# Performance work log

Hardware: AMD Instinct MI355X
Metric: run time of the kernel (lower is better)

Reference implementation:

```python
import jax, jax.numpy as jnp
import numpy as np

N, E, DIN, DOUT, DE = 100000, 250000, 32, 32, 13


def setup_inputs() -> dict:
    key = jax.random.key(0)
    ks = jax.random.split(key, 10)
    def u(k, shape, fan):
        b = 1.0 / np.sqrt(fan)
        return jax.random.uniform(k, shape, jnp.float32, -b, b)
    x = jax.random.normal(ks[0], (N, DIN), jnp.float32)
    edge_index = jax.random.randint(ks[1], (2, E), 0, N)
    edge_attr = jax.random.uniform(ks[2], (E, DE), jnp.float32)
    # NNConv's edge network: Linear(DE -> DIN*DOUT)
    nn_w = u(ks[3], (DIN * DOUT, DE), DE)
    nn_b = u(ks[4], (DIN * DOUT,), DE)
    # NNConv root weight + bias
    root = u(ks[5], (DIN, DOUT), DIN)
    bias = jnp.zeros((DOUT,), jnp.float32)
    # GRU(input=DIN, hidden=DOUT), single layer, seq_len=1
    w_ih = u(ks[6], (3 * DOUT, DIN), DOUT)
    w_hh = u(ks[7], (3 * DOUT, DOUT), DOUT)
    b_ih = u(ks[8], (3 * DOUT,), DOUT)
    b_hh = u(ks[9], (3 * DOUT,), DOUT)
    return dict(x=x, edge_attr=edge_attr, nn_w=nn_w, nn_b=nn_b, root=root,
                bias=bias, w_ih=w_ih, w_hh=w_hh, b_ih=b_ih, b_hh=b_hh,
                edge_index=edge_index)


def reference(x, edge_attr, nn_w, nn_b, root, bias, w_ih, w_hh, b_ih, b_hh, edge_index):
    identity = x
    h0 = x  # h is None -> h = x.unsqueeze(0); squeeze the seq dim here
    # norm='_None' (identity) and Dropout in eval mode (identity)
    src, dst = edge_index[0], edge_index[1]
    # NNConv: per-edge weight matrix from edge_attr  [E, DIN, DOUT]
    W = (edge_attr @ nn_w.T + nn_b).reshape(E, DIN, DOUT)
    msg = jnp.einsum('ei,eio->eo', x[src], W)           # [E, DOUT]
    agg = jax.ops.segment_sum(msg, dst, num_segments=N)  # [N, DOUT]
    cnt = jax.ops.segment_sum(jnp.ones((E, 1), x.dtype), dst, num_segments=N)
    mean = agg / jnp.maximum(cnt, 1.0)                   # aggr='mean'
    conv = mean + x @ root + bias
    # celu then GRU step (seq_len=1)
    c = jax.nn.celu(conv)
    gi = c @ w_ih.T + b_ih
    gh = h0 @ w_hh.T + b_hh
    ir, iz, ic = jnp.split(gi, 3, axis=1)
    hr, hz, hc = jnp.split(gh, 3, axis=1)
    r = jax.nn.sigmoid(ir + hr)
    z = jax.nn.sigmoid(iz + hz)
    n = jnp.tanh(ic + r * hc)
    h_new = (1.0 - z) * n + z * h0
    out = jax.nn.relu(h_new + identity)  # res=True, act=ReLU
    return out, h_new[None]
```

## Files before the change

kernel.cpp:

```cpp
#include <hip/hip_runtime.h>
#include <hip/hip_bf16.h>
#include <stdint.h>

#define DIN 32
#define DOUT 32
#define DE 13

typedef float f32x4 __attribute__((ext_vector_type(4)));
typedef short s16x8 __attribute__((ext_vector_type(8)));
typedef int   i32x4 __attribute__((ext_vector_type(4)));

__device__ __forceinline__ float bf2f(unsigned short u) {
    return __uint_as_float(((uint32_t)u) << 16);
}
__device__ __forceinline__ unsigned short f2bf(float f) {
    uint32_t b = __float_as_uint(f);
    b += 0x7FFFu + ((b >> 16) & 1u);
    return (unsigned short)(b >> 16);
}
__device__ __forceinline__ uint32_t pk2(float a, float b) {
    float2 t; t.x = a; t.y = b;
    __hip_bfloat162 h = __float22bfloat162_rn(t);
    return *(uint32_t*)&h;
}
__device__ __forceinline__ float sigm(float v) { return 1.f / (1.f + __expf(-v)); }
__device__ __forceinline__ float tanh_fast(float v) { return 2.f / (1.f + __expf(-2.f * v)) - 1.f; }

#define KE_LDS (28 * 512)
__global__ __launch_bounds__(256) void kE(const float* __restrict__ x,
        const float* __restrict__ ea, const int* __restrict__ ei,
        const float* __restrict__ nn_w, const float* __restrict__ nn_b,
        __hip_bfloat162* __restrict__ agg, float* __restrict__ cnt, int E) {
    __shared__ unsigned short Al[KE_LDS];
    __shared__ uint32_t tr4[4][256];
    const int tid = threadIdx.x;
    for (int t = tid; t < KE_LDS; t += 256) {
        int j = t & 7;
        int lane = (t >> 3) & 63;
        int tile = t >> 9;
        int at2 = tile >= 14 ? 1 : 0;
        int kt = tile - at2 * 14;
        int o = at2 * 16 + (lane & 15);
        int i = ((lane >> 4) << 3) + j;
        float v = (kt < 13) ? nn_w[(i * 32 + o) * 13 + kt] : nn_b[i * 32 + o];
        Al[t] = f2bf(v);
    }
    __syncthreads();
    const int lane = tid & 63;
    const int wv = tid >> 6;
    const int el = lane & 15;
    const int quad = lane >> 4;
    const int q8 = quad << 3;
    uint32_t* trw = &tr4[wv][0];
    const int wave = (blockIdx.x * 256 + tid) >> 6;
    const int nw = (gridDim.x * 256) >> 6;
    const int nstrips = E >> 4;
    for (int s = wave; s < nstrips; s += nw) {
        const int e = (s << 4) + el;
        const int srcv = ei[e];
        const int dstv = ei[E + e];
        const float* eab = ea + (size_t)(s << 4) * 13;
        #pragma unroll
        for (int t = 0; t < 4; ++t) {
            int idx = t * 64 + lane;
            if (idx < 208) trw[idx] = __float_as_uint(eab[idx]);
        }
        const float* xq = x + (size_t)srcv * 32 + q8;
        f32x4 xlo = *(const f32x4*)xq;
        f32x4 xhi = *(const f32x4*)(xq + 4);
        i32x4 bi;
        bi[0] = pk2(xlo[0], xlo[1]);
        bi[1] = pk2(xlo[2], xlo[3]);
        bi[2] = pk2(xhi[0], xhi[1]);
        bi[3] = pk2(xhi[2], xhi[3]);
        s16x8 bfr = __builtin_bit_cast(s16x8, bi);
        float g[14];
        #pragma unroll
        for (int d = 0; d < 13; ++d) g[d] = __uint_as_float(trw[el * 13 + d]);
        g[13] = 1.0f;
        f32x4 acc0 = {0.f, 0.f, 0.f, 0.f}, acc1 = {0.f, 0.f, 0.f, 0.f};
        const f32x4 zz = {0.f, 0.f, 0.f, 0.f};
        #pragma unroll
        for (int kt = 0; kt < 14; ++kt) {
            s16x8 a0 = *(const s16x8*)&Al[kt * 512 + lane * 8];
            s16x8 a1 = *(const s16x8*)&Al[(14 + kt) * 512 + lane * 8];
            f32x4 y0 = __builtin_amdgcn_mfma_f32_16x16x32_bf16(a0, bfr, zz, 0, 0, 0);
            f32x4 y1 = __builtin_amdgcn_mfma_f32_16x16x32_bf16(a1, bfr, zz, 0, 0, 0);
            float gk = g[kt];
            #pragma unroll
            for (int r = 0; r < 4; ++r) {
                acc0[r] = fmaf(gk, y0[r], acc0[r]);
                acc1[r] = fmaf(gk, y1[r], acc1[r]);
            }
        }
        {
            uint2 p0, p1;
            p0.x = pk2(acc0[0], acc0[1]); p0.y = pk2(acc0[2], acc0[3]);
            p1.x = pk2(acc1[0], acc1[1]); p1.y = pk2(acc1[2], acc1[3]);
            *(uint2*)&trw[el * 16 + quad * 2] = p0;
            *(uint2*)&trw[el * 16 + 8 + quad * 2] = p1;
        }
        #pragma unroll
        for (int p = 0; p < 4; ++p) {
            int e4 = (p << 2) + quad;
            uint32_t val = trw[e4 * 16 + el];
            int d4 = __shfl(dstv, e4, 64);
            __hip_bfloat162 hv = *(__hip_bfloat162*)&val;
            unsafeAtomicAdd(&agg[(size_t)d4 * 16 + el], hv);
        }
        if (lane < 16) atomicAdd(&cnt[dstv], 1.0f);
    }
}

__global__ __launch_bounds__(256) void kF(const float* __restrict__ x,
        const __hip_bfloat16* __restrict__ aggb, const float* __restrict__ cnt,
        const float* __restrict__ root, const float* __restrict__ bias,
        const float* __restrict__ w_ih, const float* __restrict__ w_hh,
        const float* __restrict__ b_ih, const float* __restrict__ b_hh,
        float* __restrict__ out, float* __restrict__ hnew, int N) {
    __shared__ __align__(16) char smem[30720];
    unsigned short* Bl = (unsigned short*)smem;
    float* scr = (float*)(smem + 14336);
    unsigned short* clds = (unsigned short*)(smem + 14336);
    const int tid = threadIdx.x;
    {
        *(f32x4*)&scr[tid * 4] = *(const f32x4*)&root[tid * 4];
        #pragma unroll
        for (int it = 0; it < 3; ++it)
            *(f32x4*)&scr[1024 + it * 1024 + tid * 4] =
                *(const f32x4*)&w_ih[0 * 0 + it * 1024 + tid * 4 - 0 * 0] * 0.f +
                *(const f32x4*)&w_hh[it * 1024 + tid * 4];
    }
    __syncthreads();
    for (int t = tid; t < 8 * 512; t += 256) {
        int j = t & 7;
        int ln = (t >> 3) & 63;
        int tt = t >> 9;
        int i = ((ln >> 4) << 3) + j;
        int c = ln & 15;
        int col = tt * 16 + c;
        float v = (col < 32) ? scr[i * 32 + col] : scr[1024 + (col - 32) * 32 + i];
        Bl[t] = f2bf(v);
    }
    __syncthreads();
    #pragma unroll
    for (int it = 0; it < 3; ++it)
        *(f32x4*)&scr[it * 1024 + tid * 4] = *(const f32x4*)&w_ih[it * 1024 + tid * 4];
    __syncthreads();
    for (int t = tid + 8 * 512; t < 14 * 512; t += 256) {
        int j = t & 7;
        int ln = (t >> 3) & 63;
        int tt = t >> 9;
        int i = ((ln >> 4) << 3) + j;
        int c = ln & 15;
        Bl[t] = f2bf(scr[((tt - 8) * 16 + c) * 32 + i]);
    }
    __syncthreads();
    const int lane = tid & 63;
    const int wv = tid >> 6;
    const int c15 = lane & 15;
    const int rowb = (lane >> 4) << 2;
    unsigned short* cl = clds + wv * 512;
    float binit[14];
    #pragma unroll
    for (int t = 0; t < 2; ++t) binit[t] = bias[t * 16 + c15];
    #pragma unroll
    for (int t = 2; t < 8; ++t) binit[t] = b_hh[t * 16 + c15 - 32];
    #pragma unroll
    for (int u = 0; u < 6; ++u) binit[8 + u] = b_ih[u * 16 + c15];
    int wave = (blockIdx.x * 256 + tid) >> 6;
    const int nw = (gridDim.x * 256) >> 6;
    const int nstrips = N >> 4;
    for (int s = wave; s < nstrips; s += nw) {
        const int n0 = s << 4;
        const float* xp = x + (size_t)(n0 + c15) * 32 + ((lane >> 4) << 3);
        f32x4 x0 = *(const f32x4*)xp;
        f32x4 x1 = *(const f32x4*)(xp + 4);
        float xr[4][2], ag[4][2], cn[4];
        #pragma unroll
        for (int r = 0; r < 4; ++r) {
            const int n = n0 + rowb + r;
            cn[r] = cnt[n];
            #pragma unroll
            for (int t = 0; t < 2; ++t) {
                xr[r][t] = x[(size_t)n * 32 + t * 16 + c15];
                ag[r][t] = bf2f(*(const unsigned short*)&aggb[(size_t)n * 32 + t * 16 + c15]);
            }
        }
        s16x8 a;
        a[0] = (short)f2bf(x0[0]); a[1] = (short)f2bf(x0[1]);
        a[2] = (short)f2bf(x0[2]); a[3] = (short)f2bf(x0[3]);
        a[4] = (short)f2bf(x1[0]); a[5] = (short)f2bf(x1[1]);
        a[6] = (short)f2bf(x1[2]); a[7] = (short)f2bf(x1[3]);
        f32x4 D[8];
        #pragma unroll
        for (int t = 0; t < 8; ++t) {
            s16x8 b = *(const s16x8*)&Bl[(t * 64 + lane) * 8];
            f32x4 ci = {binit[t], binit[t], binit[t], binit[t]};
            D[t] = __builtin_amdgcn_mfma_f32_16x16x32_bf16(a, b, ci, 0, 0, 0);
        }
        #pragma unroll
        for (int r = 0; r < 4; ++r) {
            float icn = 1.f / fmaxf(cn[r], 1.f);
            #pragma unroll
            for (int t = 0; t < 2; ++t) {
                float conv = ag[r][t] * icn + D[t][r];
                float cv = conv > 0.f ? conv : (__expf(conv) - 1.f);
                cl[(rowb + r) * 32 + t * 16 + c15] = f2bf(cv);
            }
        }
        s16x8 a2 = *(const s16x8*)&cl[c15 * 32 + ((lane >> 4) << 3)];
        f32x4 G[6];
        #pragma unroll
        for (int u = 0; u < 6; ++u) {
            s16x8 b = *(const s16x8*)&Bl[((8 + u) * 64 + lane) * 8];
            f32x4 ci = {binit[8 + u], binit[8 + u], binit[8 + u], binit[8 + u]};
            G[u] = __builtin_amdgcn_mfma_f32_16x16x32_bf16(a2, b, ci, 0, 0, 0);
        }
        #pragma unroll
        for (int t = 0; t < 2; ++t) {
            #pragma unroll
            for (int r = 0; r < 4; ++r) {
                float rg = sigm(G[t][r] + D[2 + t][r]);
                float z  = sigm(G[2 + t][r] + D[4 + t][r]);
                float nn = tanh_fast(G[4 + t][r] + rg * D[6 + t][r]);
                float h  = (1.f - z) * nn + z * xr[r][t];
                float ov = h + xr[r][t];
                size_t oi = (size_t)(n0 + rowb + r) * 32 + t * 16 + c15;
                out[oi]  = ov > 0.f ? ov : 0.f;
                hnew[oi] = h;
            }
        }
    }
}

extern "C" void kernel_launch(void* const* d_in, const int* in_sizes, int n_in,
                              void* d_out, int out_size, void* d_ws, size_t ws_size,
                              hipStream_t stream) {
    const float* x    = (const float*)d_in[0];
    const float* ea   = (const float*)d_in[1];
    const float* nn_w = (const float*)d_in[2];
    const float* nn_b = (const float*)d_in[3];
    const float* root = (const float*)d_in[4];
    const float* bias = (const float*)d_in[5];
    const float* w_ih = (const float*)d_in[6];
    const float* w_hh = (const float*)d_in[7];
    const float* b_ih = (const float*)d_in[8];
    const float* b_hh = (const float*)d_in[9];
    const int*   ei   = (const int*)d_in[10];
    const int N = in_sizes[0] / DIN;
    const int E = in_sizes[10] / 2;
    float* out  = (float*)d_out;
    float* hnew = out + (size_t)N * DOUT;

    const size_t agg_bytes = (size_t)N * 32 * sizeof(__hip_bfloat16);

    __hip_bfloat162* agg = (__hip_bfloat162*)d_ws;
    float* cnt = (float*)((char*)d_ws + agg_bytes);
    kE<<<1024, 256, 0, stream>>>(x, ea, ei, nn_w, nn_b, agg, cnt, E);
    kF<<<768, 256, 0, stream>>>(x, (const __hip_bfloat16*)d_ws, cnt, root, bias,
                                w_ih, w_hh, b_ih, b_hh, out, hnew, N);
}
```

Measured before the change: 146.6 us.

## Replicate scatter accumulators per XCC and reduce replicas in the node kernel

The edge kernel reads the hardware XCC id and sends its bf16 aggregate and count atomics into a per-XCC replica of the accumulator buffers. It issues them as raw non-returning global atomics, which keeps each atomic inside the local XCC's L2 instead of contending across dies. The node kernel then sums all 8 replicas when it loads each node's aggregate and count. The packed layout changes so the two halves of the output pair into one 32-bit word. This trades eight times the workspace and extra reads in the node kernel for less cross-die atomic traffic, and falls back to a single replica if the workspace is too small.

```diff
diff --git a/kernel.cpp b/kernel.cpp
--- a/kernel.cpp
+++ b/kernel.cpp
@@ -9,6 +9,7 @@
 typedef float f32x4 __attribute__((ext_vector_type(4)));
 typedef short s16x8 __attribute__((ext_vector_type(8)));
 typedef int   i32x4 __attribute__((ext_vector_type(4)));
+typedef unsigned int u32x4 __attribute__((ext_vector_type(4)));
 
 __device__ __forceinline__ float bf2f(unsigned short u) {
     return __uint_as_float(((uint32_t)u) << 16);
@@ -27,13 +28,25 @@
 __device__ __forceinline__ float tanh_fast(float v) { return 2.f / (1.f + __expf(-2.f * v)) - 1.f; }
 
 #define KE_LDS (28 * 512)
+template<bool LOCAL>
 __global__ __launch_bounds__(256) void kE(const float* __restrict__ x,
         const float* __restrict__ ea, const int* __restrict__ ei,
         const float* __restrict__ nn_w, const float* __restrict__ nn_b,
-        __hip_bfloat162* __restrict__ agg, float* __restrict__ cnt, int E) {
+        uint32_t* __restrict__ agg, float* __restrict__ cnt, int E, int N) {
     __shared__ unsigned short Al[KE_LDS];
     __shared__ uint32_t tr4[4][256];
     const int tid = threadIdx.x;
+
+    uint32_t* aggx = agg;
+    float*    cntx = cnt;
+    if (LOCAL) {
+        uint32_t xcc;
+        asm("s_getreg_b32 %0, hwreg(HW_REG_XCC_ID)" : "=s"(xcc));
+        xcc &= 7u;
+        aggx = agg + (size_t)xcc * ((size_t)N * 16);
+        cntx = cnt + (size_t)xcc * (size_t)N;
+    }
+
     for (int t = tid; t < KE_LDS; t += 256) {
         int j = t & 7;
         int lane = (t >> 3) & 63;
@@ -94,26 +107,45 @@
             }
         }
         {
-            uint2 p0, p1;
-            p0.x = pk2(acc0[0], acc0[1]); p0.y = pk2(acc0[2], acc0[3]);
-            p1.x = pk2(acc1[0], acc1[1]); p1.y = pk2(acc1[2], acc1[3]);
-            *(uint2*)&trw[el * 16 + quad * 2] = p0;
-            *(uint2*)&trw[el * 16 + 8 + quad * 2] = p1;
+            u32x4 pw;
+            pw[0] = pk2(acc0[0], acc1[0]);
+            pw[1] = pk2(acc0[1], acc1[1]);
+            pw[2] = pk2(acc0[2], acc1[2]);
+            pw[3] = pk2(acc0[3], acc1[3]);
+            *(u32x4*)&trw[el * 16 + quad * 4] = pw;
         }
         #pragma unroll
         for (int p = 0; p < 4; ++p) {
             int e4 = (p << 2) + quad;
             uint32_t val = trw[e4 * 16 + el];
             int d4 = __shfl(dstv, e4, 64);
-            __hip_bfloat162 hv = *(__hip_bfloat162*)&val;
-            unsafeAtomicAdd(&agg[(size_t)d4 * 16 + el], hv);
-        }
-        if (lane < 16) atomicAdd(&cnt[dstv], 1.0f);
-    }
-}
-
+            if (LOCAL) {
+                uint32_t* pa = aggx + (size_t)d4 * 16 + el;
+                asm volatile("global_atomic_pk_add_bf16 %0, %1, off"
+                             :: "v"(pa), "v"(val) : "memory");
+            } else {
+                __hip_bfloat162 hv = *(__hip_bfloat162*)&val;
+                unsafeAtomicAdd((__hip_bfloat162*)(aggx + (size_t)d4 * 16 + el), hv);
+            }
+        }
+        if (lane < 16) {
+            if (LOCAL) {
+                float* pc = cntx + dstv;
+                asm volatile("global_atomic_add_f32 %0, %1, off"
+                             :: "v"(pc), "v"(1.0f) : "memory");
+            } else {
+                atomicAdd(&cntx[dstv], 1.0f);
+            }
+        }
+    }
+    if (LOCAL) {
+        asm volatile("s_waitcnt vmcnt(0)" ::: "memory");
+    }
+}
+
+template<int NREP>
 __global__ __launch_bounds__(256) void kF(const float* __restrict__ x,
-        const __hip_bfloat16* __restrict__ aggb, const float* __restrict__ cnt,
+        const uint32_t* __restrict__ aggw, const float* __restrict__ cnt,
         const float* __restrict__ root, const float* __restrict__ bias,
         const float* __restrict__ w_ih, const float* __restrict__ w_hh,
         const float* __restrict__ b_ih, const float* __restrict__ b_hh,
@@ -178,14 +210,26 @@
         f32x4 x1 = *(const f32x4*)(xp + 4);
         float xr[4][2], ag[4][2], cn[4];
         #pragma unroll
+        for (int r = 0; r < 4; ++r) { ag[r][0] = 0.f; ag[r][1] = 0.f; cn[r] = 0.f; }
+        #pragma unroll
+        for (int q = 0; q < NREP; ++q) {
+            const uint32_t* aw = aggw + (size_t)q * ((size_t)N * 16);
+            const float* cq = cnt + (size_t)q * N;
+            #pragma unroll
+            for (int r = 0; r < 4; ++r) {
+                const int n = n0 + rowb + r;
+                uint32_t w = aw[(size_t)n * 16 + c15];
+                ag[r][0] += bf2f((unsigned short)(w & 0xFFFFu));
+                ag[r][1] += bf2f((unsigned short)(w >> 16));
+                cn[r] += cq[n];
+            }
+        }
+        #pragma unroll
         for (int r = 0; r < 4; ++r) {
             const int n = n0 + rowb + r;
-            cn[r] = cnt[n];
-            #pragma unroll
-            for (int t = 0; t < 2; ++t) {
+            #pragma unroll
+            for (int t = 0; t < 2; ++t)
                 xr[r][t] = x[(size_t)n * 32 + t * 16 + c15];
-                ag[r][t] = bf2f(*(const unsigned short*)&aggb[(size_t)n * 32 + t * 16 + c15]);
-            }
         }
         s16x8 a;
         a[0] = (short)f2bf(x0[0]); a[1] = (short)f2bf(x0[1]);
@@ -253,11 +297,20 @@
     float* out  = (float*)d_out;
     float* hnew = out + (size_t)N * DOUT;
 
-    const size_t agg_bytes = (size_t)N * 32 * sizeof(__hip_bfloat16);
-
-    __hip_bfloat162* agg = (__hip_bfloat162*)d_ws;
-    float* cnt = (float*)((char*)d_ws + agg_bytes);
-    kE<<<1024, 256, 0, stream>>>(x, ea, ei, nn_w, nn_b, agg, cnt, E);
-    kF<<<768, 256, 0, stream>>>(x, (const __hip_bfloat16*)d_ws, cnt, root, bias,
-                                w_ih, w_hh, b_ih, b_hh, out, hnew, N);
-}
+    const size_t aggB = (size_t)N * 16 * sizeof(uint32_t);
+    const size_t cntB = (size_t)N * sizeof(float);
+    const bool rep8 = ws_size >= 8 * (aggB + cntB);
+    const int nrep = rep8 ? 8 : 1;
+
+    uint32_t* agg = (uint32_t*)d_ws;
+    float* cnt = (float*)((char*)d_ws + (size_t)nrep * aggB);
+    if (rep8) {
+        kE<true><<<1024, 256, 0, stream>>>(x, ea, ei, nn_w, nn_b, agg, cnt, E, N);
+        kF<8><<<768, 256, 0, stream>>>(x, agg, cnt, root, bias,
+                                       w_ih, w_hh, b_ih, b_hh, out, hnew, N);
+    } else {
+        kE<false><<<1024, 256, 0, stream>>>(x, ea, ei, nn_w, nn_b, agg, cnt, E, N);
+        kF<1><<<768, 256, 0, stream>>>(x, agg, cnt, root, bias,
+                                       w_ih, w_hh, b_ih, b_hh, out, hnew, N);
+    }
+}
```

Result: slower. 168.7 us (+15.1%).

## Software-pipeline edge kernel with double-buffered LDS and prefetched indices/features

Applied to the files above, without the earlier changes.

Restructures the edge kernel loop into a software pipeline. Edge indices are fetched two strips ahead, edge attributes one strip ahead through registers into a double-buffered LDS slot, and the next strip's source features are loaded before the atomics are issued. The bias tile now seeds the accumulators instead of running through the FMA loop, and the aggregate is packed so each bf16x2 word holds columns c and c+16. The node kernel reads that word with a single 32-bit load. Launch bounds add an occupancy hint and the node kernel grid grows; the extra registers and LDS could cut occupancy.

```diff
diff --git a/kernel.cpp b/kernel.cpp
--- a/kernel.cpp
+++ b/kernel.cpp
@@ -9,6 +9,7 @@
 typedef float f32x4 __attribute__((ext_vector_type(4)));
 typedef short s16x8 __attribute__((ext_vector_type(8)));
 typedef int   i32x4 __attribute__((ext_vector_type(4)));
+typedef unsigned int u32x4 __attribute__((ext_vector_type(4)));
 
 __device__ __forceinline__ float bf2f(unsigned short u) {
     return __uint_as_float(((uint32_t)u) << 16);
@@ -27,12 +28,12 @@
 __device__ __forceinline__ float tanh_fast(float v) { return 2.f / (1.f + __expf(-2.f * v)) - 1.f; }
 
 #define KE_LDS (28 * 512)
-__global__ __launch_bounds__(256) void kE(const float* __restrict__ x,
+__global__ __launch_bounds__(256, 4) void kE(const float* __restrict__ x,
         const float* __restrict__ ea, const int* __restrict__ ei,
         const float* __restrict__ nn_w, const float* __restrict__ nn_b,
-        __hip_bfloat162* __restrict__ agg, float* __restrict__ cnt, int E) {
+        uint32_t* __restrict__ agg, float* __restrict__ cnt, int E) {
     __shared__ unsigned short Al[KE_LDS];
-    __shared__ uint32_t tr4[4][256];
+    __shared__ uint32_t trD[4][2][256];
     const int tid = threadIdx.x;
     for (int t = tid; t < KE_LDS; t += 256) {
         int j = t & 7;
@@ -51,42 +52,86 @@
     const int el = lane & 15;
     const int quad = lane >> 4;
     const int q8 = quad << 3;
-    uint32_t* trw = &tr4[wv][0];
     const int wave = (blockIdx.x * 256 + tid) >> 6;
     const int nw = (gridDim.x * 256) >> 6;
     const int nstrips = E >> 4;
-    for (int s = wave; s < nstrips; s += nw) {
-        const int e = (s << 4) + el;
-        const int srcv = ei[e];
-        const int dstv = ei[E + e];
-        const float* eab = ea + (size_t)(s << 4) * 13;
+    int sC = wave;
+    if (sC >= nstrips) return;
+    int sN = sC + nw, sNN = sN + nw;
+
+    const int eC = (sC << 4) + el;
+    const int srcC = ei[eC];
+    int dstC = ei[E + eC];
+    int srcN = 0, dstN = 0;
+    if (sN < nstrips) {
+        const int e1 = (sN << 4) + el;
+        srcN = ei[e1];
+        dstN = ei[E + e1];
+    }
+    {
+        const float* eab = ea + (size_t)(sC << 4) * 13;
         #pragma unroll
         for (int t = 0; t < 4; ++t) {
             int idx = t * 64 + lane;
-            if (idx < 208) trw[idx] = __float_as_uint(eab[idx]);
-        }
-        const float* xq = x + (size_t)srcv * 32 + q8;
-        f32x4 xlo = *(const f32x4*)xq;
-        f32x4 xhi = *(const f32x4*)(xq + 4);
+            if (idx < 208) trD[wv][0][idx] = __float_as_uint(eab[idx]);
+        }
+    }
+    uint32_t eaR[4] = {0u, 0u, 0u, 0u};
+    if (sN < nstrips) {
+        const float* eab = ea + (size_t)(sN << 4) * 13;
+        #pragma unroll
+        for (int t = 0; t < 4; ++t) {
+            int idx = t * 64 + lane;
+            eaR[t] = (idx < 208) ? __float_as_uint(eab[idx]) : 0u;
+        }
+    }
+    const float* xq0 = x + (size_t)srcC * 32 + q8;
+    f32x4 xlo = *(const f32x4*)xq0;
+    f32x4 xhi = *(const f32x4*)(xq0 + 4);
+
+    int pb = 0;
+    const f32x4 zz = {0.f, 0.f, 0.f, 0.f};
+    for (;;) {
+        const bool hasN  = sN  < nstrips;
+        const bool hasNN = sNN < nstrips;
+        int srcNN = 0, dstNN = 0;
+        if (hasNN) {
+            const int e2 = (sNN << 4) + el;
+            srcNN = ei[e2];
+            dstNN = ei[E + e2];
+        }
+        if (hasN) {
+            #pragma unroll
+            for (int t = 0; t < 4; ++t) {
+                int idx = t * 64 + lane;
+                if (idx < 208) trD[wv][pb ^ 1][idx] = eaR[t];
+            }
+        }
+        if (hasNN) {
+            const float* eab = ea + (size_t)(sNN << 4) * 13;
+            #pragma unroll
+            for (int t = 0; t < 4; ++t) {
+                int idx = t * 64 + lane;
+                eaR[t] = (idx < 208) ? __float_as_uint(eab[idx]) : 0u;
+            }
+        }
         i32x4 bi;
         bi[0] = pk2(xlo[0], xlo[1]);
         bi[1] = pk2(xlo[2], xlo[3]);
         bi[2] = pk2(xhi[0], xhi[1]);
         bi[3] = pk2(xhi[2], xhi[3]);
         s16x8 bfr = __builtin_bit_cast(s16x8, bi);
-        float g[14];
-        #pragma unroll
-        for (int d = 0; d < 13; ++d) g[d] = __uint_as_float(trw[el * 13 + d]);
-        g[13] = 1.0f;
-        f32x4 acc0 = {0.f, 0.f, 0.f, 0.f}, acc1 = {0.f, 0.f, 0.f, 0.f};
-        const f32x4 zz = {0.f, 0.f, 0.f, 0.f};
-        #pragma unroll
-        for (int kt = 0; kt < 14; ++kt) {
+        s16x8 aB0 = *(const s16x8*)&Al[13 * 512 + lane * 8];
+        s16x8 aB1 = *(const s16x8*)&Al[27 * 512 + lane * 8];
+        f32x4 acc0 = __builtin_amdgcn_mfma_f32_16x16x32_bf16(aB0, bfr, zz, 0, 0, 0);
+        f32x4 acc1 = __builtin_amdgcn_mfma_f32_16x16x32_bf16(aB1, bfr, zz, 0, 0, 0);
+        #pragma unroll
+        for (int kt = 0; kt < 13; ++kt) {
             s16x8 a0 = *(const s16x8*)&Al[kt * 512 + lane * 8];
             s16x8 a1 = *(const s16x8*)&Al[(14 + kt) * 512 + lane * 8];
             f32x4 y0 = __builtin_amdgcn_mfma_f32_16x16x32_bf16(a0, bfr, zz, 0, 0, 0);
             f32x4 y1 = __builtin_amdgcn_mfma_f32_16x16x32_bf16(a1, bfr, zz, 0, 0, 0);
-            float gk = g[kt];
+            float gk = __uint_as_float(trD[wv][pb][el * 13 + kt]);
             #pragma unroll
             for (int r = 0; r < 4; ++r) {
                 acc0[r] = fmaf(gk, y0[r], acc0[r]);
@@ -94,26 +139,43 @@
             }
         }
         {
-            uint2 p0, p1;
-            p0.x = pk2(acc0[0], acc0[1]); p0.y = pk2(acc0[2], acc0[3]);
-            p1.x = pk2(acc1[0], acc1[1]); p1.y = pk2(acc1[2], acc1[3]);
-            *(uint2*)&trw[el * 16 + quad * 2] = p0;
-            *(uint2*)&trw[el * 16 + 8 + quad * 2] = p1;
-        }
+            u32x4 pw;
+            pw[0] = pk2(acc0[0], acc1[0]);
+            pw[1] = pk2(acc0[1], acc1[1]);
+            pw[2] = pk2(acc0[2], acc1[2]);
+            pw[3] = pk2(acc0[3], acc1[3]);
+            *(u32x4*)&trD[wv][pb][el * 16 + quad * 4] = pw;
+        }
+        uint32_t v4s[4];
+        int dd[4];
         #pragma unroll
         for (int p = 0; p < 4; ++p) {
             int e4 = (p << 2) + quad;
-            uint32_t val = trw[e4 * 16 + el];
-            int d4 = __shfl(dstv, e4, 64);
-            __hip_bfloat162 hv = *(__hip_bfloat162*)&val;
-            unsafeAtomicAdd(&agg[(size_t)d4 * 16 + el], hv);
-        }
-        if (lane < 16) atomicAdd(&cnt[dstv], 1.0f);
-    }
-}
-
-__global__ __launch_bounds__(256) void kF(const float* __restrict__ x,
-        const __hip_bfloat16* __restrict__ aggb, const float* __restrict__ cnt,
+            v4s[p] = trD[wv][pb][e4 * 16 + el];
+            dd[p] = __shfl(dstC, e4, 64);
+        }
+        if (hasN) {
+            const float* xq = x + (size_t)srcN * 32 + q8;
+            xlo = *(const f32x4*)xq;
+            xhi = *(const f32x4*)(xq + 4);
+        }
+        __builtin_amdgcn_sched_barrier(0);
+        #pragma unroll
+        for (int p = 0; p < 4; ++p) {
+            __hip_bfloat162 hv = *(__hip_bfloat162*)&v4s[p];
+            unsafeAtomicAdd((__hip_bfloat162*)&agg[(size_t)dd[p] * 16 + el], hv);
+        }
+        if (lane < 16) atomicAdd(&cnt[dstC], 1.0f);
+        __builtin_amdgcn_sched_barrier(0);
+        if (!hasN) break;
+        sC = sN; sN = sNN; sNN += nw;
+        dstC = dstN; srcN = srcNN; dstN = dstNN;
+        pb ^= 1;
+    }
+}
+
+__global__ __launch_bounds__(256, 4) void kF(const float* __restrict__ x,
+        const uint32_t* __restrict__ aggw, const float* __restrict__ cnt,
         const float* __restrict__ root, const float* __restrict__ bias,
         const float* __restrict__ w_ih, const float* __restrict__ w_hh,
         const float* __restrict__ b_ih, const float* __restrict__ b_hh,
@@ -128,7 +190,6 @@
         #pragma unroll
         for (int it = 0; it < 3; ++it)
             *(f32x4*)&scr[1024 + it * 1024 + tid * 4] =
-                *(const f32x4*)&w_ih[0 * 0 + it * 1024 + tid * 4 - 0 * 0] * 0.f +
                 *(const f32x4*)&w_hh[it * 1024 + tid * 4];
     }
     __syncthreads();
@@ -180,12 +241,13 @@
         #pragma unroll
         for (int r = 0; r < 4; ++r) {
             const int n = n0 + rowb + r;
+            uint32_t w = aggw[(size_t)n * 16 + c15];
+            ag[r][0] = bf2f((unsigned short)(w & 0xFFFFu));
+            ag[r][1] = bf2f((unsigned short)(w >> 16));
             cn[r] = cnt[n];
             #pragma unroll
-            for (int t = 0; t < 2; ++t) {
+            for (int t = 0; t < 2; ++t)
                 xr[r][t] = x[(size_t)n * 32 + t * 16 + c15];
-                ag[r][t] = bf2f(*(const unsigned short*)&aggb[(size_t)n * 32 + t * 16 + c15]);
-            }
         }
         s16x8 a;
         a[0] = (short)f2bf(x0[0]); a[1] = (short)f2bf(x0[1]);
@@ -253,11 +315,11 @@
     float* out  = (float*)d_out;
     float* hnew = out + (size_t)N * DOUT;
 
-    const size_t agg_bytes = (size_t)N * 32 * sizeof(__hip_bfloat16);
-
-    __hip_bfloat162* agg = (__hip_bfloat162*)d_ws;
+    const size_t agg_bytes = (size_t)N * 16 * sizeof(uint32_t);
+
+    uint32_t* agg = (uint32_t*)d_ws;
     float* cnt = (float*)((char*)d_ws + agg_bytes);
     kE<<<1024, 256, 0, stream>>>(x, ea, ei, nn_w, nn_b, agg, cnt, E);
-    kF<<<768, 256, 0, stream>>>(x, (const __hip_bfloat16*)d_ws, cnt, root, bias,
-                                w_ih, w_hh, b_ih, b_hh, out, hnew, N);
-}
+    kF<<<1024, 256, 0, stream>>>(x, agg, cnt, root, bias,
+                                 w_ih, w_hh, b_ih, b_hh, out, hnew, N);
+}
```

After: 147.8 us. No clear change (+0.8%).
